# Kernel tuning notes

Hardware: AMD Instinct MI355X
Metric: run time of the kernel (lower is better)

Reference implementation:

```python
import jax, jax.numpy as jnp
import numpy as np

D_MODEL = 1024
H = 16
D_K = D_MODEL // H
MASK_VALUE = -2000000000.0  # fp32 path in the original module


def setup_inputs() -> dict:
    key = jax.random.key(0)
    ks = jax.random.split(key, 7)
    B, S = 2, 2048
    scale = 1.0 / np.sqrt(D_MODEL)
    inp = {
        "q": jax.random.normal(ks[0], (B, S, D_MODEL), jnp.float32),
        "k": jax.random.normal(ks[1], (B, S, D_MODEL), jnp.float32),
        "v": jax.random.normal(ks[2], (B, S, D_MODEL), jnp.float32),
        # causal mask, broadcast over batch and heads
        "mask": jnp.tril(jnp.ones((1, 1, S, S), jnp.int32)),
        "w_q": jax.random.normal(ks[3], (D_MODEL, D_MODEL), jnp.float32) * scale,
        "w_k": jax.random.normal(ks[4], (D_MODEL, D_MODEL), jnp.float32) * scale,
        "w_v": jax.random.normal(ks[5], (D_MODEL, D_MODEL), jnp.float32) * scale,
        "w_o": jax.random.normal(ks[6], (D_MODEL, D_MODEL), jnp.float32) * scale,
    }
    return inp


def reference(q, k, v, mask, w_q, w_k, w_v, w_o):
    B, S, _ = q.shape
    # Linear(d_model, d_model, bias=False): x @ W.T  (weights stored [out, in])
    def proj(x, w):
        y = jnp.einsum('bsd,ed->bse', x, w)
        return y.reshape(B, -1, H, D_K).transpose(0, 2, 1, 3)  # [B, H, S, d_k]

    Q = proj(q, w_q)
    K = proj(k, w_k)
    V = proj(v, w_v)

    scores = jnp.einsum('bhsd,bhtd->bhst', Q, K) * (D_K ** -0.5)  # [B,H,S,S]
    scores = jnp.where(mask == 0, MASK_VALUE, scores)
    attn = jax.nn.softmax(scores, axis=-1)
    x = jnp.einsum('bhst,bhtd->bhsd', attn, V)                     # [B,H,S,d_k]
    x = x.transpose(0, 2, 1, 3).reshape(B, -1, D_MODEL)            # [B,S,d_model]
    return jnp.einsum('bsd,ed->bse', x, w_o)
```

## Files before the change

kernel.cpp:

```cpp
#include <hip/hip_runtime.h>
#include <math.h>

#define S_LEN 2048
#define DM 1024
#define NH 16
#define DK 64
#define BATCH 2
#define MS (BATCH*S_LEN)

typedef __attribute__((ext_vector_type(8))) short bf16x8;
typedef __attribute__((ext_vector_type(4))) float f32x4;
typedef __attribute__((ext_vector_type(16))) float f32x16;
typedef unsigned short u16;
typedef unsigned int u32;

__device__ __forceinline__ u16 f2b(float f) {
  union { float f; u32 u; } x; x.f = f;
  u32 r = x.u + 0x7FFFu + ((x.u >> 16) & 1u);
  return (u16)(r >> 16);
}

__device__ __forceinline__ u32 cvtpk_bf16(float lo, float hi) {
  u32 r;
  asm volatile("v_cvt_pk_bf16_f32 %0, %1, %2" : "=v"(r) : "v"(lo), "v"(hi));
  return r;
}

struct CvtArgs {
  const float* src[7];
  u16* dst[7];
  float scl[7];
  int n4[7];
};

__global__ void cvt_all(CvtArgs a) {
  const int seg = blockIdx.y;
  const float* __restrict__ in = a.src[seg];
  u16* __restrict__ out = a.dst[seg];
  const float s = a.scl[seg];
  const int n4 = a.n4[seg];
  int idx = blockIdx.x * blockDim.x + threadIdx.x;
  int stride = gridDim.x * blockDim.x;
  for (int i = idx; i < n4; i += stride) {
    float4 v = ((const float4*)in)[i];
    ushort4 o;
    o.x = f2b(v.x * s); o.y = f2b(v.y * s); o.z = f2b(v.z * s); o.w = f2b(v.w * s);
    ((ushort4*)out)[i] = o;
  }
}

__device__ __forceinline__ void gload_lds16(const u16* g, u16* l) {
  __builtin_amdgcn_global_load_lds((const __attribute__((address_space(1))) u32*)g,
                                   (__attribute__((address_space(3))) u32*)l, 16, 0, 0);
}

template<bool OUT_BF16, int BM>
__device__ __forceinline__ void gemm_body(
    const u16* __restrict__ A, const u16* __restrict__ B, void* __restrict__ Cout,
    int M, int N, int K, int bx, int by, u16* lsA, u16* lsB)
{
  constexpr int MF = BM / 32;
  const int tid = threadIdx.x;
  const int lane = tid & 63;
  const int wid = tid >> 6;
  const int wr = wid >> 1, wc = wid & 1;
  const int m0 = by * BM, n0 = bx * 128;

  f32x4 acc[MF][4];
#pragma unroll
  for (int i = 0; i < MF; ++i)
#pragma unroll
    for (int j = 0; j < 4; ++j) acc[i][j] = (f32x4){0.f, 0.f, 0.f, 0.f};

  const int ntiles = K >> 5;

#pragma unroll
  for (int i = 0; i < BM/64; ++i) {
    int u = tid + i * 256;
    gload_lds16(A + (size_t)(m0 + (u >> 2)) * K + (u & 3) * 8, &lsA[u * 8]);
  }
#pragma unroll
  for (int i = 0; i < 2; ++i) {
    int u = tid + i * 256;
    gload_lds16(B + (size_t)(n0 + (u >> 2)) * K + (u & 3) * 8, &lsB[u * 8]);
  }

  for (int kt = 0; kt < ntiles; ++kt) {
    __syncthreads();
    bf16x8 af[MF], bfr[4];
    const int kOff = (lane >> 4) * 8;
#pragma unroll
    for (int m = 0; m < MF; ++m)
      af[m] = *(const bf16x8*)&lsA[(wr * (BM/2) + m * 16 + (lane & 15)) * 32 + kOff];
#pragma unroll
    for (int n = 0; n < 4; ++n)
      bfr[n] = *(const bf16x8*)&lsB[(wc * 64 + n * 16 + (lane & 15)) * 32 + kOff];
    __syncthreads();
    if (kt + 1 < ntiles) {
      int k0 = (kt + 1) << 5;
#pragma unroll
      for (int i = 0; i < BM/64; ++i) {
        int u = tid + i * 256;
        gload_lds16(A + (size_t)(m0 + (u >> 2)) * K + k0 + (u & 3) * 8, &lsA[u * 8]);
      }
#pragma unroll
      for (int i = 0; i < 2; ++i) {
        int u = tid + i * 256;
        gload_lds16(B + (size_t)(n0 + (u >> 2)) * K + k0 + (u & 3) * 8, &lsB[u * 8]);
      }
    }
#pragma unroll
    for (int m = 0; m < MF; ++m)
#pragma unroll
      for (int n = 0; n < 4; ++n)
        acc[m][n] = __builtin_amdgcn_mfma_f32_16x16x32_bf16(af[m], bfr[n], acc[m][n], 0, 0, 0);
  }

  const int rbase = m0 + wr * (BM/2) + ((lane >> 4) << 2);
  const int cbase = n0 + wc * 64 + (lane & 15);
#pragma unroll
  for (int m = 0; m < MF; ++m)
#pragma unroll
    for (int n = 0; n < 4; ++n)
#pragma unroll
      for (int j = 0; j < 4; ++j) {
        int r = rbase + m * 16 + j;
        int c = cbase + n * 16;
        if (OUT_BF16)
          ((u16*)Cout)[(size_t)r * N + c] = f2b(acc[m][n][j]);
        else
          ((float*)Cout)[(size_t)r * N + c] = acc[m][n][j];
      }
}

struct G3Args {
  const u16* A[3];
  const u16* B[3];
  u16* C[3];
};

__global__ __launch_bounds__(256) void gemm_qkv(G3Args g) {
  __shared__ u16 lsA[128*32];
  __shared__ u16 lsB[128*32];
  const int bid = blockIdx.x;
  int gi, f;
  if (bid < 512) {
    int sbid = (bid & 7) * 64 + (bid >> 3);
    gi = sbid >> 8;
    f = sbid & 255;
  } else {
    gi = 2;
    f = bid - 512;
  }
  const int gx = (gi == 2) ? 32 : 8;
  const int N = (gi == 2) ? MS : DM;
  const int M = (gi == 2) ? DM : MS;
  gemm_body<true,128>(g.A[gi], g.B[gi], g.C[gi], M, N, DM,
                      f % gx, f / gx, lsA, lsB);
}

__global__ __launch_bounds__(256) void gemm_out(
    const u16* __restrict__ A, const u16* __restrict__ B, float* __restrict__ C) {
  __shared__ u16 lsA[64*32];
  __shared__ u16 lsB[128*32];
  const int bid = blockIdx.x;
  int sbid = (bid & 7) * 64 + (bid >> 3);
  gemm_body<false,64>(A, B, C, MS, DM, DM, sbid & 7, sbid >> 3, lsA, lsB);
}

__global__ __launch_bounds__(256) void attn_fwd(
    const u16* __restrict__ Qp, const u16* __restrict__ Kp, const u16* __restrict__ Vt,
    u16* __restrict__ AO)
{
  __shared__ __align__(16) u16 lds_kv[4][4096];
  __shared__ float lds_l[4][2][32];
  const int tid = threadIdx.x;
  const int lane = tid & 63;
  const int w = tid >> 6;
  const int ql = lane & 31;
  const int h = lane >> 5;
  const int bid = blockIdx.x;
  const int j = 63 - (bid >> 5);
  const int bh = bid & 31;
  const int b = bh >> 4;
  const int hh = bh & 15;
  const int q0 = j * 32;
  const int qg = q0 + ql;
  const size_t baseQK = (size_t)b * S_LEN * DM + hh * DK;
  const size_t baseV  = (size_t)hh * DK * MS + (size_t)b * S_LEN;

  u16* const lk = lds_kv[w];
  u16* const lv = lds_kv[w] + 2048;

  bf16x8 qf[4];
#pragma unroll
  for (int ks = 0; ks < 4; ++ks)
    qf[ks] = *(const bf16x8*)&Qp[baseQK + (size_t)qg * DM + ks * 16 + h * 8];
  asm volatile("s_waitcnt vmcnt(0)" ::: "memory");

  f32x16 ot[2];
#pragma unroll
  for (int n = 0; n < 2; ++n)
#pragma unroll
    for (int r = 0; r < 16; ++r) ot[n][r] = 0.f;
  float lrun = 0.f;

  const u16* kptr[4];
  const u16* vptr[4];
#pragma unroll
  for (int jj = 0; jj < 4; ++jj) {
    int c = jj * 64 + lane;
    int kr = c >> 3, kc = c & 7;
    kptr[jj] = Kp + baseQK + (size_t)(w * 32 + kr) * DM + (kc ^ (kr & 7)) * 8;
    int vr = c >> 2, vc = c & 3;
    vptr[jj] = Vt + baseV + (size_t)vr * MS + w * 32 + (vc ^ (vr & 3)) * 8;
  }

#define STAGE_K() do { \
    _Pragma("unroll") \
    for (int jj = 0; jj < 4; ++jj) { \
      int c = jj * 64 + lane; \
      gload_lds16(kptr[jj], &lk[c * 8]); \
      kptr[jj] += (size_t)128 * DM; \
    } \
  } while (0)

#define STAGE_V() do { \
    _Pragma("unroll") \
    for (int jj = 0; jj < 4; ++jj) { \
      int c = jj * 64 + lane; \
      gload_lds16(vptr[jj], &lv[c * 8]); \
      vptr[jj] += 128; \
    } \
  } while (0)

  if (w <= j) { STAGE_K(); STAGE_V(); }

  for (int tt = w; tt <= j; tt += 4) {
    const bool nx = (tt + 4 <= j);
    asm volatile("s_waitcnt vmcnt(4)" ::: "memory");
    bf16x8 kf[4];
#pragma unroll
    for (int ks = 0; ks < 4; ++ks)
      kf[ks] = *(const bf16x8*)&lk[(ql * 8 + ((2 * ks + h) ^ (ql & 7))) * 8];
    asm volatile("s_waitcnt lgkmcnt(0)" ::: "memory");
    if (nx) STAGE_K();

    f32x16 st;
#pragma unroll
    for (int r = 0; r < 16; ++r) st[r] = 0.f;
    __builtin_amdgcn_s_setprio(1);
#pragma unroll
    for (int ks = 0; ks < 4; ++ks)
      st = __builtin_amdgcn_mfma_f32_32x32x16_bf16(kf[ks], qf[ks], st, 0, 0, 0);
    __builtin_amdgcn_s_setprio(0);

    if (tt == j) {
#pragma unroll
      for (int r = 0; r < 16; ++r) {
        int kvg = tt * 32 + (r & 3) + 8 * (r >> 2) + 4 * h;
        if (kvg > qg) st[r] = -1e30f;
      }
    }

#pragma unroll
    for (int r = 0; r < 16; ++r) {
      float p_ = st[r];
      asm("v_exp_f32 %0, %1" : "=v"(p_) : "v"(p_));
      st[r] = p_;
    }
    {
      float t0 = st[0] + st[1], t1 = st[2] + st[3];
      float t2 = st[4] + st[5], t3 = st[6] + st[7];
      float t4 = st[8] + st[9], t5 = st[10] + st[11];
      float t6 = st[12] + st[13], t7 = st[14] + st[15];
      float u0 = t0 + t1, u1 = t2 + t3, u2 = t4 + t5, u3 = t6 + t7;
      lrun += (u0 + u1) + (u2 + u3);
    }

    if (nx) { asm volatile("s_waitcnt vmcnt(4)" ::: "memory"); }
    else    { asm volatile("s_waitcnt vmcnt(0)" ::: "memory"); }
    bf16x8 vf[2][2];
#pragma unroll
    for (int n = 0; n < 2; ++n)
#pragma unroll
      for (int kst = 0; kst < 2; ++kst)
        vf[n][kst] = *(const bf16x8*)&lv[((n * 32 + ql) * 4 + ((2 * kst + h) ^ (ql & 3))) * 8];
    asm volatile("s_waitcnt lgkmcnt(0)" ::: "memory");
    if (nx) STAGE_V();

#pragma unroll
    for (int kst = 0; kst < 2; ++kst) {
      u32 pkg[4];
#pragma unroll
      for (int g4 = 0; g4 < 4; ++g4)
        pkg[g4] = cvtpk_bf16(st[8 * kst + 2 * g4], st[8 * kst + 2 * g4 + 1]);
      asm("v_permlane32_swap_b32 %0, %1" : "+v"(pkg[0]), "+v"(pkg[2]));
      asm("v_permlane32_swap_b32 %0, %1" : "+v"(pkg[1]), "+v"(pkg[3]));
      union { u32 u[4]; bf16x8 v; } pb;
      pb.u[0] = pkg[0]; pb.u[1] = pkg[1]; pb.u[2] = pkg[2]; pb.u[3] = pkg[3];
      __builtin_amdgcn_s_setprio(1);
#pragma unroll
      for (int n = 0; n < 2; ++n)
        ot[n] = __builtin_amdgcn_mfma_f32_32x32x16_bf16(vf[n][kst], pb.v, ot[n], 0, 0, 0);
      __builtin_amdgcn_s_setprio(0);
    }
  }

  lds_l[w][h][ql] = lrun;

  {
    float* comb = (float*)lds_kv[w];
#pragma unroll
    for (int n = 0; n < 2; ++n)
#pragma unroll
      for (int r = 0; r < 16; ++r) {
        int d = 32 * n + (r & 3) + 8 * (r >> 2) + 4 * h;
        comb[d * 32 + (ql ^ (d & 31))] = ot[n][r];
      }
  }
  __syncthreads();
  {
    const int q = tid >> 3;
    const int d0 = (tid & 7) * 8;
    float lsum = 0.f;
#pragma unroll
    for (int w2 = 0; w2 < 4; ++w2)
      lsum += lds_l[w2][0][q] + lds_l[w2][1][q];
    float inv = 1.0f / lsum;
    const float* c0 = (const float*)lds_kv[0];
    const float* c1 = (const float*)lds_kv[1];
    const float* c2 = (const float*)lds_kv[2];
    const float* c3 = (const float*)lds_kv[3];
    u32 o4[4];
#pragma unroll
    for (int ii = 0; ii < 4; ++ii) {
      int da = d0 + 2 * ii, db = da + 1;
      int ia = da * 32 + (q ^ (da & 31));
      int ib = db * 32 + (q ^ (db & 31));
      float va = c0[ia] + c1[ia] + c2[ia] + c3[ia];
      float vb = c0[ib] + c1[ib] + c2[ib] + c3[ib];
      o4[ii] = cvtpk_bf16(va * inv, vb * inv);
    }
    uint4 outv;
    outv.x = o4[0]; outv.y = o4[1]; outv.z = o4[2]; outv.w = o4[3];
    *(uint4*)&AO[baseQK + (size_t)(q0 + q) * DM + d0] = outv;
  }
#undef STAGE_K
#undef STAGE_V
}

extern "C" void kernel_launch(void* const* d_in, const int* in_sizes, int n_in,
                              void* d_out, int out_size, void* d_ws, size_t ws_size,
                              hipStream_t stream) {
  const float* q  = (const float*)d_in[0];
  const float* k  = (const float*)d_in[1];
  const float* v  = (const float*)d_in[2];
  const float* wq = (const float*)d_in[4];
  const float* wk = (const float*)d_in[5];
  const float* wv = (const float*)d_in[6];
  const float* wo = (const float*)d_in[7];

  const size_t nIn = (size_t)MS * DM;
  const size_t nW  = (size_t)DM * DM;

  u16* ws = (u16*)d_ws;
  u16* qb  = ws; ws += nIn;
  u16* kb  = ws; ws += nIn;
  u16* vb  = ws; ws += nIn;
  u16* wqb = ws; ws += nW;
  u16* wkb = ws; ws += nW;
  u16* wvb = ws; ws += nW;
  u16* wob = ws; ws += nW;
  u16* Qp  = ws; ws += nIn;
  u16* Kp  = ws; ws += nIn;
  u16* Vt  = ws; ws += nIn;
  u16* AO  = ws; ws += nIn;

  CvtArgs ca;
  const float QSCL = 0.125f * 1.44269504089f;
  ca.src[0] = q;  ca.dst[0] = qb;  ca.n4[0] = (int)(nIn / 4); ca.scl[0] = 1.f;
  ca.src[1] = k;  ca.dst[1] = kb;  ca.n4[1] = (int)(nIn / 4); ca.scl[1] = 1.f;
  ca.src[2] = v;  ca.dst[2] = vb;  ca.n4[2] = (int)(nIn / 4); ca.scl[2] = 1.f;
  ca.src[3] = wq; ca.dst[3] = wqb; ca.n4[3] = (int)(nW / 4);  ca.scl[3] = QSCL;
  ca.src[4] = wk; ca.dst[4] = wkb; ca.n4[4] = (int)(nW / 4);  ca.scl[4] = 1.f;
  ca.src[5] = wv; ca.dst[5] = wvb; ca.n4[5] = (int)(nW / 4);  ca.scl[5] = 1.f;
  ca.src[6] = wo; ca.dst[6] = wob; ca.n4[6] = (int)(nW / 4);  ca.scl[6] = 1.f;
  cvt_all<<<dim3(256, 7), 256, 0, stream>>>(ca);

  G3Args g3;
  g3.A[0] = qb;  g3.B[0] = wqb; g3.C[0] = Qp;
  g3.A[1] = kb;  g3.B[1] = wkb; g3.C[1] = Kp;
  g3.A[2] = wvb; g3.B[2] = vb;  g3.C[2] = Vt;
  gemm_qkv<<<dim3(768), 256, 0, stream>>>(g3);

  attn_fwd<<<dim3(64 * 32), 256, 0, stream>>>(Qp, Kp, Vt, AO);

  gemm_out<<<dim3(512), 256, 0, stream>>>(AO, wob, (float*)d_out);
}
```

Baseline: 115.4 us.

## Fuse fp32-to-bf16 activation conversion into QKV GEMM tile loads

The separate conversion pass for the q, k and v activations is removed. The QKV GEMM now loads fp32 tiles directly into LDS with an XOR swizzle and converts them to bf16 when reading fragments, so the conversion kernel only handles the weights. This drops a full read and write of three activation tensors plus bf16 staging buffers. In exchange the GEMM moves twice the bytes per tile, uses more LDS, and does conversion ALU work inside the main loop.

Result: slower. 122.7 us (+6.4%).

```diff
diff --git a/kernel.cpp b/kernel.cpp
--- a/kernel.cpp
+++ b/kernel.cpp
@@ -27,10 +27,10 @@
 }
 
 struct CvtArgs {
-  const float* src[7];
-  u16* dst[7];
-  float scl[7];
-  int n4[7];
+  const float* src[4];
+  u16* dst[4];
+  float scl[4];
+  int n4[4];
 };
 
 __global__ void cvt_all(CvtArgs a) {
@@ -54,9 +54,9 @@
                                    (__attribute__((address_space(3))) u32*)l, 16, 0, 0);
 }
 
-template<bool OUT_BF16, int BM>
+template<bool OUT_BF16, int BM, bool AF32, bool BF32>
 __device__ __forceinline__ void gemm_body(
-    const u16* __restrict__ A, const u16* __restrict__ B, void* __restrict__ Cout,
+    const void* __restrict__ Av, const void* __restrict__ Bv, void* __restrict__ Cout,
     int M, int N, int K, int bx, int by, u16* lsA, u16* lsB)
 {
   constexpr int MF = BM / 32;
@@ -74,47 +74,86 @@
 
   const int ntiles = K >> 5;
 
-#pragma unroll
-  for (int i = 0; i < BM/64; ++i) {
-    int u = tid + i * 256;
-    gload_lds16(A + (size_t)(m0 + (u >> 2)) * K + (u & 3) * 8, &lsA[u * 8]);
-  }
-#pragma unroll
-  for (int i = 0; i < 2; ++i) {
-    int u = tid + i * 256;
-    gload_lds16(B + (size_t)(n0 + (u >> 2)) * K + (u & 3) * 8, &lsB[u * 8]);
-  }
-
+#define GSTAGE(K0) do { \
+    if constexpr (AF32) { \
+      _Pragma("unroll") \
+      for (int i = 0; i < BM/32; ++i) { \
+        int u = tid + i * 256; \
+        int row = u >> 3, c8 = u & 7; \
+        gload_lds16((const u16*)((const float*)Av + (size_t)(m0 + row) * K + (K0) + ((c8 ^ (row & 7)) << 2)), &lsA[u * 8]); \
+      } \
+    } else { \
+      _Pragma("unroll") \
+      for (int i = 0; i < BM/64; ++i) { \
+        int u = tid + i * 256; \
+        gload_lds16((const u16*)Av + (size_t)(m0 + (u >> 2)) * K + (K0) + (u & 3) * 8, &lsA[u * 8]); \
+      } \
+    } \
+    if constexpr (BF32) { \
+      _Pragma("unroll") \
+      for (int i = 0; i < 4; ++i) { \
+        int u = tid + i * 256; \
+        int row = u >> 3, c8 = u & 7; \
+        gload_lds16((const u16*)((const float*)Bv + (size_t)(n0 + row) * K + (K0) + ((c8 ^ (row & 7)) << 2)), &lsB[u * 8]); \
+      } \
+    } else { \
+      _Pragma("unroll") \
+      for (int i = 0; i < 2; ++i) { \
+        int u = tid + i * 256; \
+        gload_lds16((const u16*)Bv + (size_t)(n0 + (u >> 2)) * K + (K0) + (u & 3) * 8, &lsB[u * 8]); \
+      } \
+    } \
+  } while (0)
+
+  GSTAGE(0);
   for (int kt = 0; kt < ntiles; ++kt) {
     __syncthreads();
     bf16x8 af[MF], bfr[4];
     const int kOff = (lane >> 4) * 8;
-#pragma unroll
-    for (int m = 0; m < MF; ++m)
-      af[m] = *(const bf16x8*)&lsA[(wr * (BM/2) + m * 16 + (lane & 15)) * 32 + kOff];
-#pragma unroll
-    for (int n = 0; n < 4; ++n)
-      bfr[n] = *(const bf16x8*)&lsB[(wc * 64 + n * 16 + (lane & 15)) * 32 + kOff];
+    const int cc = (lane >> 4) * 2;
+#pragma unroll
+    for (int m = 0; m < MF; ++m) {
+      int row = wr * (BM/2) + m * 16 + (lane & 15);
+      if constexpr (AF32) {
+        const float* sA = (const float*)lsA;
+        f32x4 a0 = *(const f32x4*)&sA[(row * 8 + (cc ^ (row & 7))) * 4];
+        f32x4 a1 = *(const f32x4*)&sA[(row * 8 + ((cc + 1) ^ (row & 7))) * 4];
+        union { u32 u[4]; bf16x8 v; } t;
+        t.u[0] = cvtpk_bf16(a0[0], a0[1]);
+        t.u[1] = cvtpk_bf16(a0[2], a0[3]);
+        t.u[2] = cvtpk_bf16(a1[0], a1[1]);
+        t.u[3] = cvtpk_bf16(a1[2], a1[3]);
+        af[m] = t.v;
+      } else {
+        af[m] = *(const bf16x8*)&lsA[row * 32 + kOff];
+      }
+    }
+#pragma unroll
+    for (int n = 0; n < 4; ++n) {
+      int row = wc * 64 + n * 16 + (lane & 15);
+      if constexpr (BF32) {
+        const float* sB = (const float*)lsB;
+        f32x4 b0 = *(const f32x4*)&sB[(row * 8 + (cc ^ (row & 7))) * 4];
+        f32x4 b1 = *(const f32x4*)&sB[(row * 8 + ((cc + 1) ^ (row & 7))) * 4];
+        union { u32 u[4]; bf16x8 v; } t;
+        t.u[0] = cvtpk_bf16(b0[0], b0[1]);
+        t.u[1] = cvtpk_bf16(b0[2], b0[3]);
+        t.u[2] = cvtpk_bf16(b1[0], b1[1]);
+        t.u[3] = cvtpk_bf16(b1[2], b1[3]);
+        bfr[n] = t.v;
+      } else {
+        bfr[n] = *(const bf16x8*)&lsB[row * 32 + kOff];
+      }
+    }
     __syncthreads();
-    if (kt + 1 < ntiles) {
-      int k0 = (kt + 1) << 5;
-#pragma unroll
-      for (int i = 0; i < BM/64; ++i) {
-        int u = tid + i * 256;
-        gload_lds16(A + (size_t)(m0 + (u >> 2)) * K + k0 + (u & 3) * 8, &lsA[u * 8]);
-      }
-#pragma unroll
-      for (int i = 0; i < 2; ++i) {
-        int u = tid + i * 256;
-        gload_lds16(B + (size_t)(n0 + (u >> 2)) * K + k0 + (u & 3) * 8, &lsB[u * 8]);
-      }
-    }
+    if (kt + 1 < ntiles) GSTAGE((kt + 1) << 5);
 #pragma unroll
     for (int m = 0; m < MF; ++m)
 #pragma unroll
       for (int n = 0; n < 4; ++n)
         acc[m][n] = __builtin_amdgcn_mfma_f32_16x16x32_bf16(af[m], bfr[n], acc[m][n], 0, 0, 0);
   }
+#undef GSTAGE
 
   const int rbase = m0 + wr * (BM/2) + ((lane >> 4) << 2);
   const int cbase = n0 + wc * 64 + (lane & 15);
@@ -134,29 +173,27 @@
 }
 
 struct G3Args {
-  const u16* A[3];
-  const u16* B[3];
-  u16* C[3];
+  const float* Aq; const float* Ak;
+  const u16* Bq;  const u16* Bk;
+  const u16* Awv; const float* Bv;
+  u16* Cq; u16* Ck; u16* Cvt;
 };
 
 __global__ __launch_bounds__(256) void gemm_qkv(G3Args g) {
-  __shared__ u16 lsA[128*32];
-  __shared__ u16 lsB[128*32];
+  __shared__ __align__(16) u16 ls[12288];
   const int bid = blockIdx.x;
-  int gi, f;
   if (bid < 512) {
     int sbid = (bid & 7) * 64 + (bid >> 3);
-    gi = sbid >> 8;
-    f = sbid & 255;
+    int gi = sbid >> 8, f = sbid & 255;
+    gemm_body<true,128,true,false>(gi ? (const void*)g.Ak : (const void*)g.Aq,
+                                   gi ? (const void*)g.Bk : (const void*)g.Bq,
+                                   gi ? g.Ck : g.Cq, MS, DM, DM,
+                                   f & 7, f >> 3, ls, ls + 8192);
   } else {
-    gi = 2;
-    f = bid - 512;
-  }
-  const int gx = (gi == 2) ? 32 : 8;
-  const int N = (gi == 2) ? MS : DM;
-  const int M = (gi == 2) ? DM : MS;
-  gemm_body<true,128>(g.A[gi], g.B[gi], g.C[gi], M, N, DM,
-                      f % gx, f / gx, lsA, lsB);
+    int f = bid - 512;
+    gemm_body<true,128,false,true>(g.Awv, g.Bv, g.Cvt, DM, MS, DM,
+                                   f & 31, f >> 5, ls, ls + 4096);
+  }
 }
 
 __global__ __launch_bounds__(256) void gemm_out(
@@ -165,7 +202,7 @@
   __shared__ u16 lsB[128*32];
   const int bid = blockIdx.x;
   int sbid = (bid & 7) * 64 + (bid >> 3);
-  gemm_body<false,64>(A, B, C, MS, DM, DM, sbid & 7, sbid >> 3, lsA, lsB);
+  gemm_body<false,64,false,false>(A, B, C, MS, DM, DM, sbid & 7, sbid >> 3, lsA, lsB);
 }
 
 __global__ __launch_bounds__(256) void attn_fwd(
@@ -365,9 +402,6 @@
   const size_t nW  = (size_t)DM * DM;
 
   u16* ws = (u16*)d_ws;
-  u16* qb  = ws; ws += nIn;
-  u16* kb  = ws; ws += nIn;
-  u16* vb  = ws; ws += nIn;
   u16* wqb = ws; ws += nW;
   u16* wkb = ws; ws += nW;
   u16* wvb = ws; ws += nW;
@@ -379,19 +413,16 @@
 
   CvtArgs ca;
   const float QSCL = 0.125f * 1.44269504089f;
-  ca.src[0] = q;  ca.dst[0] = qb;  ca.n4[0] = (int)(nIn / 4); ca.scl[0] = 1.f;
-  ca.src[1] = k;  ca.dst[1] = kb;  ca.n4[1] = (int)(nIn / 4); ca.scl[1] = 1.f;
-  ca.src[2] = v;  ca.dst[2] = vb;  ca.n4[2] = (int)(nIn / 4); ca.scl[2] = 1.f;
-  ca.src[3] = wq; ca.dst[3] = wqb; ca.n4[3] = (int)(nW / 4);  ca.scl[3] = QSCL;
-  ca.src[4] = wk; ca.dst[4] = wkb; ca.n4[4] = (int)(nW / 4);  ca.scl[4] = 1.f;
-  ca.src[5] = wv; ca.dst[5] = wvb; ca.n4[5] = (int)(nW / 4);  ca.scl[5] = 1.f;
-  ca.src[6] = wo; ca.dst[6] = wob; ca.n4[6] = (int)(nW / 4);  ca.scl[6] = 1.f;
-  cvt_all<<<dim3(256, 7), 256, 0, stream>>>(ca);
+  ca.src[0] = wq; ca.dst[0] = wqb; ca.n4[0] = (int)(nW / 4); ca.scl[0] = QSCL;
+  ca.src[1] = wk; ca.dst[1] = wkb; ca.n4[1] = (int)(nW / 4); ca.scl[1] = 1.f;
+  ca.src[2] = wv; ca.dst[2] = wvb; ca.n4[2] = (int)(nW / 4); ca.scl[2] = 1.f;
+  ca.src[3] = wo; ca.dst[3] = wob; ca.n4[3] = (int)(nW / 4); ca.scl[3] = 1.f;
+  cvt_all<<<dim3(64, 4), 256, 0, stream>>>(ca);
 
   G3Args g3;
-  g3.A[0] = qb;  g3.B[0] = wqb; g3.C[0] = Qp;
-  g3.A[1] = kb;  g3.B[1] = wkb; g3.C[1] = Kp;
-  g3.A[2] = wvb; g3.B[2] = vb;  g3.C[2] = Vt;
+  g3.Aq = q;  g3.Ak = k;  g3.Bq = wqb; g3.Bk = wkb;
+  g3.Awv = wvb; g3.Bv = v;
+  g3.Cq = Qp; g3.Ck = Kp; g3.Cvt = Vt;
   gemm_qkv<<<dim3(768), 256, 0, stream>>>(g3);
 
   attn_fwd<<<dim3(64 * 32), 256, 0, stream>>>(Qp, Kp, Vt, AO);
```
